# Kernel optimization log

Measured on AMD Instinct MI355X. Metric: run time of the kernel, lower is better.

The kernel has to match this reference:

```python
import jax, jax.numpy as jnp
import numpy as np

B, L, D = 2, 2048, 2048
NH, HD = 16, 128
SCALE = HD ** -0.5


def setup_inputs() -> dict:
    key = jax.random.key(0)
    ks = jax.random.split(key, 9)
    s = D ** -0.5  # roughly torch Linear init scale
    return {
        "hidden_states": jax.random.normal(ks[0], (B, L, D), dtype=jnp.float32),
        "Wq": jax.random.normal(ks[1], (NH * HD, D), dtype=jnp.float32) * s,
        "bq": jnp.zeros((NH * HD,), dtype=jnp.float32),
        "Wk": jax.random.normal(ks[2], (NH * HD, D), dtype=jnp.float32) * s,
        "bk": jnp.zeros((NH * HD,), dtype=jnp.float32),
        "Wv": jax.random.normal(ks[3], (NH * HD, D), dtype=jnp.float32) * s,
        "bv": jnp.zeros((NH * HD,), dtype=jnp.float32),
        "Wo": jax.random.normal(ks[4], (D, NH * HD), dtype=jnp.float32) * s,
        "bo": jnp.zeros((D,), dtype=jnp.float32),
    }


def reference(hidden_states, Wq, bq, Wk, bk, Wv, bv, Wo, bo):
    # projections (torch Linear: x @ W.T + b), split into heads: b s h d
    q = (hidden_states @ Wq.T + bq).reshape(B, L, NH, HD)
    k = (hidden_states @ Wk.T + bk).reshape(B, L, NH, HD)
    v = (hidden_states @ Wv.T + bv).reshape(B, L, NH, HD)
    # scores: [B, NH, L, L]
    scores = jnp.einsum("bqhd,bkhd->bhqk", q, k) * SCALE
    causal = jnp.tril(jnp.ones((L, L), dtype=bool))  # True = keep
    scores = jnp.where(causal, scores, jnp.float32(-jnp.inf))
    probs = jax.nn.softmax(scores, axis=-1)
    out = jnp.einsum("bhqk,bkhd->bqhd", probs, v).reshape(B, L, NH * HD)
    return out @ Wo.T + bo
```

## Files before the change

kernel.cpp:

```cpp
#include <hip/hip_runtime.h>

#define B_  2
#define L_  2048
#define D_  2048
#define NH_ 16
#define HD_ 128

typedef __bf16 bf16_t;
typedef __bf16 bf16x8 __attribute__((ext_vector_type(8)));
typedef __bf16 bf16x4 __attribute__((ext_vector_type(4)));
typedef float  f32x4  __attribute__((ext_vector_type(4)));

typedef const __attribute__((address_space(1))) void* gas_ptr;
typedef __attribute__((address_space(3))) void* las_ptr;

__device__ __forceinline__ void g2l16(const void* g, void* l) {
    __builtin_amdgcn_global_load_lds((gas_ptr)g, (las_ptr)l, 16, 0, 0);
}

__device__ __forceinline__ void raw_barrier() {
    asm volatile("s_barrier" ::: "memory");
}
__device__ __forceinline__ void wait_vm8() {
    asm volatile("s_waitcnt vmcnt(8)" ::: "memory");
}
__device__ __forceinline__ void wait_vm4() {
    asm volatile("s_waitcnt vmcnt(4)" ::: "memory");
}
__device__ __forceinline__ void wait_vm2() {
    asm volatile("s_waitcnt vmcnt(2)" ::: "memory");
}
__device__ __forceinline__ void wait_vm0() {
    asm volatile("s_waitcnt vmcnt(0)" ::: "memory");
}

__global__ __launch_bounds__(256) void cvt_all(const float* __restrict__ X,
                                               const float* __restrict__ Wq,
                                               const float* __restrict__ Wk,
                                               const float* __restrict__ Wv,
                                               const float* __restrict__ Wo,
                                               bf16_t* __restrict__ Xb,
                                               bf16_t* __restrict__ Wqkvb,
                                               bf16_t* __restrict__ Wob) {
    int i = blockIdx.x * 256 + threadIdx.x;
    const float* src;
    bf16_t* dst;
    int off;
    if (i < 2097152) { src = X; dst = Xb; off = i; }
    else {
        int j = i - 2097152;
        int w = j >> 20;
        off = j & 1048575;
        src = (w == 0) ? Wq : (w == 1) ? Wk : (w == 2) ? Wv : Wo;
        dst = (w == 3) ? Wob : Wqkvb + (size_t)w * 4194304;
    }
    float4 v = ((const float4*)src)[off];
    bf16x4 o;
    o[0] = (bf16_t)v.x; o[1] = (bf16_t)v.y; o[2] = (bf16_t)v.z; o[3] = (bf16_t)v.w;
    ((bf16x4*)dst)[off] = o;
}

__global__ __launch_bounds__(256) void gemm_bt(const bf16_t* __restrict__ A,
                                               const bf16_t* __restrict__ Bw,
                                               const float* __restrict__ bias,
                                               float* __restrict__ C,
                                               int M, int N, int K) {
    constexpr int BK = 32;
    __shared__ __align__(16) bf16_t smem[16384];
    const int tid  = threadIdx.x;
    const int wave = tid >> 6, lane = tid & 63;
    const int quad = lane >> 4, l16 = lane & 15;
    const int tm = blockIdx.y * 128, tn = blockIdx.x * 128;
    const int wm = (wave >> 1) * 64, wn = (wave & 1) * 64;

    const int srow = wave * 16 + (lane >> 2);
    const int scol = (lane & 3) * 8;
    const bf16_t* Ag = A  + (size_t)(tm + srow) * K + scol;
    const bf16_t* Bg = Bw + (size_t)(tn + srow) * K + scol;
    const size_t rowskip = (size_t)64 * K;

    auto stage = [&](int k0, int p) {
        bf16_t* a = smem + p * 4096 + (wave * 16) * BK;
        bf16_t* bl = smem + 8192 + p * 4096 + (wave * 16) * BK;
        g2l16(Ag + k0, a);
        g2l16(Ag + k0 + rowskip, a + 64 * BK);
        g2l16(Bg + k0, bl);
        g2l16(Bg + k0 + rowskip, bl + 64 * BK);
    };

    f32x4 acc[4][4] = {};
    const int niter = K / BK;
    stage(0, 0);

    for (int i = 0; i < niter; ++i) {
        const int p = i & 1;
        if (i + 1 < niter) { stage((i + 1) * BK, p ^ 1); wait_vm4(); }
        else wait_vm0();
        raw_barrier();

        const bf16_t* Alp = smem + p * 4096;
        const bf16_t* Blp = smem + 8192 + p * 4096;
        bf16x8 af[4], bf[4];
#pragma unroll
        for (int ii = 0; ii < 4; ++ii)
            af[ii] = *(const bf16x8*)(Alp + (wm + ii * 16 + l16) * BK + quad * 8);
#pragma unroll
        for (int j = 0; j < 4; ++j)
            bf[j] = *(const bf16x8*)(Blp + (wn + j * 16 + l16) * BK + quad * 8);
#pragma unroll
        for (int ii = 0; ii < 4; ++ii)
#pragma unroll
            for (int j = 0; j < 4; ++j)
                acc[ii][j] = __builtin_amdgcn_mfma_f32_16x16x32_bf16(af[ii], bf[j], acc[ii][j], 0, 0, 0);
        raw_barrier();
    }

#pragma unroll
    for (int j = 0; j < 4; ++j) {
        const int col = tn + wn + j * 16 + l16;
        const float bv = bias[col];
#pragma unroll
        for (int i = 0; i < 4; ++i) {
            const int row0 = tm + wm + i * 16 + quad * 4;
#pragma unroll
            for (int r = 0; r < 4; ++r)
                C[(size_t)(row0 + r) * N + col] = acc[i][j][r] + bv;
        }
    }
}

__global__ __launch_bounds__(512, 2) void gemm_qkv(const bf16_t* __restrict__ A,
                                                   const bf16_t* __restrict__ Bw,
                                                   const float* __restrict__ b0,
                                                   const float* __restrict__ b1,
                                                   const float* __restrict__ b2,
                                                   bf16_t* __restrict__ QK,
                                                   bf16_t* __restrict__ Vt) {
    constexpr int K  = D_;
    constexpr int BK = 64;
    constexpr int NT = K / BK;
    __shared__ __align__(16) bf16_t smem[65536];

    const int tid  = threadIdx.x;
    const int wave = tid >> 6, lane = tid & 63;
    const int quad = lane >> 4, l16 = lane & 15;
    const int tm = blockIdx.y * 256, tn = blockIdx.x * 256;
    const int wm = (wave >> 2) * 128;
    const int wn = (wave & 3) * 64;
    const int seg = tn >> 11;

    const int srow = tid >> 3;
    const int sg   = (tid & 7) ^ (srow & 7);
    const bf16_t* Ag = A  + (size_t)(tm + srow) * K + sg * 8;
    const bf16_t* Bg = Bw + (size_t)(tn + srow) * K + sg * 8;
    const int ldsw = wave * 512;

    auto stageA = [&](int t, int h) {
        bf16_t* l = smem + (t & 1) * 32768 + h * 8192 + ldsw;
        const bf16_t* g = Ag + (size_t)h * 128 * K + t * BK;
        g2l16(g, l);
        g2l16(g + (size_t)64 * K, l + 4096);
    };
    auto stageB = [&](int t, int h) {
        bf16_t* l = smem + (t & 1) * 32768 + 16384 + h * 8192 + ldsw;
        const bf16_t* g = Bg + (size_t)h * 128 * K + t * BK;
        g2l16(g, l);
        g2l16(g + (size_t)64 * K, l + 4096);
    };

    f32x4 acc[8][4] = {};

    stageA(0, 0); stageA(0, 1); stageB(0, 0); stageB(0, 1);

    const int abase_w = (wave >> 2) * 8192;
    const int bbase_w = 16384 + ((wave >> 1) & 1) * 8192;
    const int brow0   = (wave & 1) * 64;

    for (int t = 0; t < NT; ++t) {
        const int p = t & 1;
        const bf16_t* Ah = smem + p * 32768 + abase_w;
        const bf16_t* Bh = smem + p * 32768 + bbase_w;
        bf16x8 af[4][2], bfr[2][2], bfr2[2][2];

        raw_barrier();
        if (t + 1 < NT) { stageA(t + 1, 0); wait_vm2(); }
        else wait_vm0();
        raw_barrier();

#pragma unroll
        for (int mb = 0; mb < 4; ++mb)
#pragma unroll
            for (int ks = 0; ks < 2; ++ks) {
                const int row = mb * 16 + l16;
                af[mb][ks] = *(const bf16x8*)(Ah + row * 64 + (((ks * 4 + quad) ^ (row & 7)) << 3));
            }
#pragma unroll
        for (int nb = 0; nb < 2; ++nb)
#pragma unroll
            for (int ks = 0; ks < 2; ++ks) {
                const int row = brow0 + nb * 16 + l16;
                bfr[nb][ks] = *(const bf16x8*)(Bh + row * 64 + (((ks * 4 + quad) ^ (row & 7)) << 3));
            }
        __builtin_amdgcn_s_setprio(1);
#pragma unroll
        for (int mb = 0; mb < 4; ++mb)
#pragma unroll
            for (int nb = 0; nb < 2; ++nb)
#pragma unroll
                for (int ks = 0; ks < 2; ++ks)
                    acc[mb][nb] = __builtin_amdgcn_mfma_f32_16x16x32_bf16(af[mb][ks], bfr[nb][ks], acc[mb][nb], 0, 0, 0);
        __builtin_amdgcn_s_setprio(0);

        if (t + 1 < NT) stageA(t + 1, 1);
#pragma unroll
        for (int nb = 0; nb < 2; ++nb)
#pragma unroll
            for (int ks = 0; ks < 2; ++ks) {
                const int row = brow0 + (nb + 2) * 16 + l16;
                bfr2[nb][ks] = *(const bf16x8*)(Bh + row * 64 + (((ks * 4 + quad) ^ (row & 7)) << 3));
            }
        raw_barrier();
        __builtin_amdgcn_s_setprio(1);
#pragma unroll
        for (int mb = 0; mb < 4; ++mb)
#pragma unroll
            for (int nb = 0; nb < 2; ++nb)
#pragma unroll
                for (int ks = 0; ks < 2; ++ks)
                    acc[mb][nb + 2] = __builtin_amdgcn_mfma_f32_16x16x32_bf16(af[mb][ks], bfr2[nb][ks], acc[mb][nb + 2], 0, 0, 0);
        __builtin_amdgcn_s_setprio(0);

        if (t + 1 < NT) stageB(t + 1, 0);
#pragma unroll
        for (int mb = 0; mb < 4; ++mb)
#pragma unroll
            for (int ks = 0; ks < 2; ++ks) {
                const int row = (mb + 4) * 16 + l16;
                af[mb][ks] = *(const bf16x8*)(Ah + row * 64 + (((ks * 4 + quad) ^ (row & 7)) << 3));
            }
        raw_barrier();
        __builtin_amdgcn_s_setprio(1);
#pragma unroll
        for (int mb = 0; mb < 4; ++mb)
#pragma unroll
            for (int nb = 0; nb < 2; ++nb)
#pragma unroll
                for (int ks = 0; ks < 2; ++ks)
                    acc[mb + 4][nb + 2] = __builtin_amdgcn_mfma_f32_16x16x32_bf16(af[mb][ks], bfr2[nb][ks], acc[mb + 4][nb + 2], 0, 0, 0);
        __builtin_amdgcn_s_setprio(0);

        if (t + 1 < NT) stageB(t + 1, 1);
#pragma unroll
        for (int nb = 0; nb < 2; ++nb)
#pragma unroll
            for (int ks = 0; ks < 2; ++ks) {
                const int row = brow0 + nb * 16 + l16;
                bfr[nb][ks] = *(const bf16x8*)(Bh + row * 64 + (((ks * 4 + quad) ^ (row & 7)) << 3));
            }
        raw_barrier();
        __builtin_amdgcn_s_setprio(1);
#pragma unroll
        for (int mb = 0; mb < 4; ++mb)
#pragma unroll
            for (int nb = 0; nb < 2; ++nb)
#pragma unroll
                for (int ks = 0; ks < 2; ++ks)
                    acc[mb + 4][nb] = __builtin_amdgcn_mfma_f32_16x16x32_bf16(af[mb][ks], bfr[nb][ks], acc[mb + 4][nb], 0, 0, 0);
        __builtin_amdgcn_s_setprio(0);
    }

    if (seg < 2) {
        const float* bias = (seg == 0) ? b0 : b1;
#pragma unroll
        for (int nb = 0; nb < 4; ++nb) {
            const int col = tn + wn + nb * 16 + l16;
            const float bv = bias[col & 2047];
#pragma unroll
            for (int mb = 0; mb < 8; ++mb) {
                const int row0 = tm + wm + mb * 16 + quad * 4;
#pragma unroll
                for (int r = 0; r < 4; ++r)
                    QK[(size_t)(row0 + r) * 4096 + col] = (bf16_t)(acc[mb][nb][r] + bv);
            }
        }
    } else {
        __syncthreads();
        bf16_t* Tw = smem + wave * 8192;
        const int colbase = (tn - 4096) + wn;
#pragma unroll
        for (int nb = 0; nb < 4; ++nb) {
            const int d = nb * 16 + l16;
            const float bv = b2[colbase + d];
#pragma unroll
            for (int mb = 0; mb < 8; ++mb)
#pragma unroll
                for (int r = 0; r < 4; ++r) {
                    const int tok = mb * 16 + quad * 4 + r;
                    Tw[d * 128 + ((((tok >> 3) ^ (d & 7)) << 3) | (tok & 7))] =
                        (bf16_t)(acc[mb][nb][r] + bv);
                }
        }
        const int dl = lane;
        const int h  = (colbase + dl) >> 7;
        const int dg = (colbase + dl) & 127;
        const int b  = tm >> 11;
        const int tokbase = (tm & 2047) + wm;
        bf16_t* gp = Vt + ((size_t)(b * NH_ + h) * HD_ + dg) * L_ + tokbase;
#pragma unroll
        for (int c = 0; c < 16; ++c) {
            bf16x8 v = *(const bf16x8*)(Tw + dl * 128 + ((c ^ (dl & 7)) << 3));
            *(bf16x8*)(gp + c * 8) = v;
        }
    }
}

__global__ __launch_bounds__(256, 2) void attn_kernel(const bf16_t* __restrict__ QK,
                                                      const bf16_t* __restrict__ Vt,
                                                      bf16_t* __restrict__ Ctx) {
    constexpr float SCALE = 0.08838834764831845f;
    constexpr float MFIX  = 8.0f;
    const int bid = blockIdx.x;
    const int bh = bid & 31;
    const int qt = 15 - (bid >> 5);
    const int b = bh >> 4, h = bh & 15;
    const int tid = threadIdx.x, wave = tid >> 6, lane = tid & 63;
    const int quad = lane >> 4, l16 = lane & 15;
    const int q0 = qt * 128;

    __shared__ bf16_t Kl[2][64 * 128];
    __shared__ bf16_t Vl[2][128 * 64];
    __shared__ bf16_t Pl[4][16 * 72];

    bf16x8 qf[2][4];
#pragma unroll
    for (int s = 0; s < 2; ++s) {
        const bf16_t* qp = QK + (size_t)(b * L_ + q0 + wave * 32 + s * 16 + l16) * 4096 + h * HD_ + quad * 8;
#pragma unroll
        for (int ks = 0; ks < 4; ++ks) qf[s][ks] = *(const bf16x8*)(qp + ks * 32);
    }

    bf16x8 ones;
#pragma unroll
    for (int j = 0; j < 8; ++j) ones[j] = (bf16_t)1.0f;

    f32x4 oacc[2][8] = {};
    f32x4 lacc[2] = {};

    const bf16_t* Kg = QK + (size_t)(b * L_) * 4096 + 2048 + h * HD_;
    const bf16_t* Vg = Vt + (size_t)(bh * HD_) * L_;

    auto stage = [&](int tile, int p) {
        const bf16_t* kg = Kg + (size_t)tile * 64 * 4096;
        const bf16_t* vg = Vg + tile * 64;
#pragma unroll
        for (int c = 0; c < 4; ++c) {
            int row = c * 16 + wave * 4 + (lane >> 4);
            int gcol = ((lane & 15) ^ (row & 15)) * 8;
            g2l16(kg + (size_t)row * 4096 + gcol, &Kl[p][(c * 16 + wave * 4) * 128]);
        }
#pragma unroll
        for (int c = 0; c < 4; ++c) {
            int row = c * 32 + wave * 8 + (lane >> 3);
            int gcol = ((lane & 7) ^ (row & 7)) * 8;
            g2l16(vg + (size_t)row * L_ + gcol, &Vl[p][(c * 32 + wave * 8) * 64]);
        }
    };

    const int n = 2 * qt + 2;
    stage(0, 0);

    for (int it = 0; it < n; ++it) {
        const int p = it & 1;
        if (it + 1 < n) {
            stage(it + 1, p ^ 1);
            wait_vm8();
        } else {
            wait_vm0();
        }
        raw_barrier();

        const int kb = it * 64;
        const bool need_mask = (it >= n - 2);

        f32x4 sa[2][4] = {};
#pragma unroll
        for (int nt = 0; nt < 4; ++nt) {
            const int krow = nt * 16 + l16;
#pragma unroll
            for (int ks = 0; ks < 4; ++ks) {
                bf16x8 kf = *(const bf16x8*)(&Kl[p][krow * 128 + (((ks * 4 + quad) ^ l16) * 8)]);
                sa[0][nt] = __builtin_amdgcn_mfma_f32_16x16x32_bf16(qf[0][ks], kf, sa[0][nt], 0, 0, 0);
                sa[1][nt] = __builtin_amdgcn_mfma_f32_16x16x32_bf16(qf[1][ks], kf, sa[1][nt], 0, 0, 0);
            }
        }

        bf16x8 pf0[2], pf1[2];
#pragma unroll
        for (int nt = 0; nt < 4; ++nt)
#pragma unroll
            for (int r = 0; r < 4; ++r) {
                float sv = sa[0][nt][r] * SCALE - MFIX;
                if (need_mask) {
                    const int key = kb + nt * 16 + l16;
                    const int qq = q0 + wave * 32 + quad * 4 + r;
                    sv = (key <= qq) ? sv : -1e30f;
                }
                Pl[wave][(quad * 4 + r) * 72 + nt * 16 + l16] = (bf16_t)__expf(sv);
            }
        pf0[0] = *(const bf16x8*)(&Pl[wave][l16 * 72 + quad * 8]);
        pf0[1] = *(const bf16x8*)(&Pl[wave][l16 * 72 + 32 + quad * 8]);

#pragma unroll
        for (int nt = 0; nt < 4; ++nt)
#pragma unroll
            for (int r = 0; r < 4; ++r) {
                float sv = sa[1][nt][r] * SCALE - MFIX;
                if (need_mask) {
                    const int key = kb + nt * 16 + l16;
                    const int qq = q0 + wave * 32 + 16 + quad * 4 + r;
                    sv = (key <= qq) ? sv : -1e30f;
                }
                Pl[wave][(quad * 4 + r) * 72 + nt * 16 + l16] = (bf16_t)__expf(sv);
            }
        pf1[0] = *(const bf16x8*)(&Pl[wave][l16 * 72 + quad * 8]);
        pf1[1] = *(const bf16x8*)(&Pl[wave][l16 * 72 + 32 + quad * 8]);

        lacc[0] = __builtin_amdgcn_mfma_f32_16x16x32_bf16(pf0[0], ones, lacc[0], 0, 0, 0);
        lacc[0] = __builtin_amdgcn_mfma_f32_16x16x32_bf16(pf0[1], ones, lacc[0], 0, 0, 0);
        lacc[1] = __builtin_amdgcn_mfma_f32_16x16x32_bf16(pf1[0], ones, lacc[1], 0, 0, 0);
        lacc[1] = __builtin_amdgcn_mfma_f32_16x16x32_bf16(pf1[1], ones, lacc[1], 0, 0, 0);

#pragma unroll
        for (int dt = 0; dt < 8; ++dt) {
            const int drow = dt * 16 + l16;
#pragma unroll
            for (int ks = 0; ks < 2; ++ks) {
                bf16x8 vf = *(const bf16x8*)(&Vl[p][drow * 64 + (((ks * 4 + quad) ^ (drow & 7)) * 8)]);
                oacc[0][dt] = __builtin_amdgcn_mfma_f32_16x16x32_bf16(pf0[ks], vf, oacc[0][dt], 0, 0, 0);
                oacc[1][dt] = __builtin_amdgcn_mfma_f32_16x16x32_bf16(pf1[ks], vf, oacc[1][dt], 0, 0, 0);
            }
        }
        raw_barrier();
    }

#pragma unroll
    for (int s = 0; s < 2; ++s)
#pragma unroll
        for (int r = 0; r < 4; ++r) {
            const float inv = 1.0f / lacc[s][r];
            const int q = q0 + wave * 32 + s * 16 + quad * 4 + r;
            bf16_t* cp = Ctx + (size_t)(b * L_ + q) * 2048 + h * HD_;
#pragma unroll
            for (int dt = 0; dt < 8; ++dt)
                cp[dt * 16 + l16] = (bf16_t)(oacc[s][dt][r] * inv);
        }
}

extern "C" void kernel_launch(void* const* d_in, const int* in_sizes, int n_in,
                              void* d_out, int out_size, void* d_ws, size_t ws_size,
                              hipStream_t stream) {
    const float* X  = (const float*)d_in[0];
    const float* Wq = (const float*)d_in[1];
    const float* bq = (const float*)d_in[2];
    const float* Wk = (const float*)d_in[3];
    const float* bk = (const float*)d_in[4];
    const float* Wv = (const float*)d_in[5];
    const float* bv = (const float*)d_in[6];
    const float* Wo = (const float*)d_in[7];
    const float* bo = (const float*)d_in[8];
    float* out = (float*)d_out;

    char* ws = (char*)d_ws;
    bf16_t* Xb   = (bf16_t*)(ws);
    bf16_t* Ctx  = (bf16_t*)(ws);
    bf16_t* Wqkv = (bf16_t*)(ws + 16777216);
    bf16_t* Wob  = (bf16_t*)(ws + 41943040);
    bf16_t* QKb  = (bf16_t*)(ws + 50331648);
    bf16_t* Vtb  = (bf16_t*)(ws + 83886080);

    cvt_all<<<24576, 256, 0, stream>>>(X, Wq, Wk, Wv, Wo, Xb, Wqkv, Wob);

    gemm_qkv<<<dim3(24, 16), 512, 0, stream>>>(Xb, Wqkv, bq, bk, bv, QKb, Vtb);

    attn_kernel<<<dim3(512), 256, 0, stream>>>(QKb, Vtb, Ctx);

    gemm_bt<<<dim3(16, 32), 256, 0, stream>>>(Ctx, Wob, bo, out,
                                              B_ * L_, D_, D_);
}
```

Measured before the change: 371.1 us.

## Split fused QKV GEMM into separate QK and V GEMM kernels

The single 24x16-block QKV projection GEMM is split into a Q/K GEMM using 256x256 tiles (256 blocks) and a new V GEMM using 256x128 tiles (256 blocks) with its own transposed-output epilogue. The goal is to fix wave quantization: 384 large blocks on 256 CUs leave a partial second wave, while two 256-block launches fill the device more evenly. The cost is an extra kernel launch, smaller tiles with less reuse in the V GEMM, and A being re-read by both kernels.

```diff
diff --git a/kernel.cpp b/kernel.cpp
--- a/kernel.cpp
+++ b/kernel.cpp
@@ -129,13 +129,11 @@
     }
 }
 
-__global__ __launch_bounds__(512, 2) void gemm_qkv(const bf16_t* __restrict__ A,
-                                                   const bf16_t* __restrict__ Bw,
-                                                   const float* __restrict__ b0,
-                                                   const float* __restrict__ b1,
-                                                   const float* __restrict__ b2,
-                                                   bf16_t* __restrict__ QK,
-                                                   bf16_t* __restrict__ Vt) {
+__global__ __launch_bounds__(512, 2) void gemm_qk(const bf16_t* __restrict__ A,
+                                                  const bf16_t* __restrict__ Bw,
+                                                  const float* __restrict__ b0,
+                                                  const float* __restrict__ b1,
+                                                  bf16_t* __restrict__ QK) {
     constexpr int K  = D_;
     constexpr int BK = 64;
     constexpr int NT = K / BK;
@@ -269,48 +267,160 @@
         __builtin_amdgcn_s_setprio(0);
     }
 
-    if (seg < 2) {
-        const float* bias = (seg == 0) ? b0 : b1;
-#pragma unroll
-        for (int nb = 0; nb < 4; ++nb) {
-            const int col = tn + wn + nb * 16 + l16;
-            const float bv = bias[col & 2047];
-#pragma unroll
-            for (int mb = 0; mb < 8; ++mb) {
-                const int row0 = tm + wm + mb * 16 + quad * 4;
-#pragma unroll
-                for (int r = 0; r < 4; ++r)
-                    QK[(size_t)(row0 + r) * 4096 + col] = (bf16_t)(acc[mb][nb][r] + bv);
-            }
-        }
-    } else {
-        __syncthreads();
-        bf16_t* Tw = smem + wave * 8192;
-        const int colbase = (tn - 4096) + wn;
-#pragma unroll
-        for (int nb = 0; nb < 4; ++nb) {
-            const int d = nb * 16 + l16;
-            const float bv = b2[colbase + d];
-#pragma unroll
-            for (int mb = 0; mb < 8; ++mb)
-#pragma unroll
-                for (int r = 0; r < 4; ++r) {
-                    const int tok = mb * 16 + quad * 4 + r;
-                    Tw[d * 128 + ((((tok >> 3) ^ (d & 7)) << 3) | (tok & 7))] =
-                        (bf16_t)(acc[mb][nb][r] + bv);
-                }
-        }
-        const int dl = lane;
-        const int h  = (colbase + dl) >> 7;
-        const int dg = (colbase + dl) & 127;
-        const int b  = tm >> 11;
-        const int tokbase = (tm & 2047) + wm;
-        bf16_t* gp = Vt + ((size_t)(b * NH_ + h) * HD_ + dg) * L_ + tokbase;
-#pragma unroll
-        for (int c = 0; c < 16; ++c) {
-            bf16x8 v = *(const bf16x8*)(Tw + dl * 128 + ((c ^ (dl & 7)) << 3));
-            *(bf16x8*)(gp + c * 8) = v;
-        }
+    const float* bias = (seg == 0) ? b0 : b1;
+#pragma unroll
+    for (int nb = 0; nb < 4; ++nb) {
+        const int col = tn + wn + nb * 16 + l16;
+        const float bv = bias[col & 2047];
+#pragma unroll
+        for (int mb = 0; mb < 8; ++mb) {
+            const int row0 = tm + wm + mb * 16 + quad * 4;
+#pragma unroll
+            for (int r = 0; r < 4; ++r)
+                QK[(size_t)(row0 + r) * 4096 + col] = (bf16_t)(acc[mb][nb][r] + bv);
+        }
+    }
+}
+
+__global__ __launch_bounds__(512, 2) void gemm_v(const bf16_t* __restrict__ A,
+                                                 const bf16_t* __restrict__ Bv,
+                                                 const float* __restrict__ b2,
+                                                 bf16_t* __restrict__ Vt) {
+    constexpr int K  = D_;
+    constexpr int BK = 64;
+    constexpr int NT = K / BK;
+    __shared__ __align__(16) bf16_t smem[49152];
+
+    const int tid  = threadIdx.x;
+    const int wave = tid >> 6, lane = tid & 63;
+    const int quad = lane >> 4, l16 = lane & 15;
+    const int hx = blockIdx.x;
+    const int tm = blockIdx.y * 256;
+    const int wm = (wave >> 1) * 64;
+    const int wn = (wave & 1) * 64;
+
+    const int srow = tid >> 3;
+    const int sg   = (tid & 7) ^ (srow & 7);
+    const bf16_t* Ag = A  + (size_t)(tm + srow) * K + sg * 8;
+    const bf16_t* Bg = Bv + (size_t)(hx * 128 + srow) * K + sg * 8;
+    const int ldsw = wave * 512;
+
+    auto stageVA = [&](int t, int q) {
+        bf16_t* l = smem + (t & 1) * 24576 + q * 4096 + ldsw;
+        g2l16(Ag + (size_t)q * 64 * K + t * BK, l);
+    };
+    auto stageVB = [&](int t, int q) {
+        bf16_t* l = smem + (t & 1) * 24576 + 16384 + q * 4096 + ldsw;
+        g2l16(Bg + (size_t)q * 64 * K + t * BK, l);
+    };
+
+    f32x4 acc[4][4] = {};
+
+    stageVA(0, 0); stageVA(0, 1); stageVA(0, 2); stageVA(0, 3);
+    stageVB(0, 0); stageVB(0, 1);
+
+    for (int t = 0; t < NT; ++t) {
+        const int p = t & 1;
+        const bf16_t* Ah = smem + p * 24576;
+        const bf16_t* Bl = smem + p * 24576 + 16384;
+        bf16x8 af0[4], af1[4], bf0[2], bf1[2], bf2[2], bf3[2];
+
+        raw_barrier();
+        if (t + 1 < NT) { stageVA(t + 1, 0); stageVA(t + 1, 1); wait_vm2(); }
+        else wait_vm0();
+        raw_barrier();
+
+#pragma unroll
+        for (int mb = 0; mb < 4; ++mb) {
+            const int row = wm + mb * 16 + l16;
+            af0[mb] = *(const bf16x8*)(Ah + row * 64 + ((quad ^ (row & 7)) << 3));
+        }
+#pragma unroll
+        for (int nb = 0; nb < 2; ++nb) {
+            const int row = wn + nb * 16 + l16;
+            bf0[nb] = *(const bf16x8*)(Bl + row * 64 + ((quad ^ (row & 7)) << 3));
+        }
+        __builtin_amdgcn_s_setprio(1);
+#pragma unroll
+        for (int mb = 0; mb < 4; ++mb)
+#pragma unroll
+            for (int nb = 0; nb < 2; ++nb)
+                acc[mb][nb] = __builtin_amdgcn_mfma_f32_16x16x32_bf16(af0[mb], bf0[nb], acc[mb][nb], 0, 0, 0);
+        __builtin_amdgcn_s_setprio(0);
+
+        if (t + 1 < NT) { stageVA(t + 1, 2); stageVB(t + 1, 0); }
+#pragma unroll
+        for (int nb = 0; nb < 2; ++nb) {
+            const int row = wn + (nb + 2) * 16 + l16;
+            bf1[nb] = *(const bf16x8*)(Bl + row * 64 + ((quad ^ (row & 7)) << 3));
+        }
+        raw_barrier();
+        __builtin_amdgcn_s_setprio(1);
+#pragma unroll
+        for (int mb = 0; mb < 4; ++mb)
+#pragma unroll
+            for (int nb = 0; nb < 2; ++nb)
+                acc[mb][nb + 2] = __builtin_amdgcn_mfma_f32_16x16x32_bf16(af0[mb], bf1[nb], acc[mb][nb + 2], 0, 0, 0);
+        __builtin_amdgcn_s_setprio(0);
+
+        if (t + 1 < NT) { stageVA(t + 1, 3); stageVB(t + 1, 1); }
+#pragma unroll
+        for (int mb = 0; mb < 4; ++mb) {
+            const int row = wm + mb * 16 + l16;
+            af1[mb] = *(const bf16x8*)(Ah + row * 64 + (((4 + quad) ^ (row & 7)) << 3));
+        }
+#pragma unroll
+        for (int nb = 0; nb < 2; ++nb) {
+            const int row = wn + (nb + 2) * 16 + l16;
+            bf2[nb] = *(const bf16x8*)(Bl + row * 64 + (((4 + quad) ^ (row & 7)) << 3));
+        }
+        raw_barrier();
+        __builtin_amdgcn_s_setprio(1);
+#pragma unroll
+        for (int mb = 0; mb < 4; ++mb)
+#pragma unroll
+            for (int nb = 0; nb < 2; ++nb)
+                acc[mb][nb + 2] = __builtin_amdgcn_mfma_f32_16x16x32_bf16(af1[mb], bf2[nb], acc[mb][nb + 2], 0, 0, 0);
+        __builtin_amdgcn_s_setprio(0);
+
+#pragma unroll
+        for (int nb = 0; nb < 2; ++nb) {
+            const int row = wn + nb * 16 + l16;
+            bf3[nb] = *(const bf16x8*)(Bl + row * 64 + (((4 + quad) ^ (row & 7)) << 3));
+        }
+        raw_barrier();
+        __builtin_amdgcn_s_setprio(1);
+#pragma unroll
+        for (int mb = 0; mb < 4; ++mb)
+#pragma unroll
+            for (int nb = 0; nb < 2; ++nb)
+                acc[mb][nb] = __builtin_amdgcn_mfma_f32_16x16x32_bf16(af1[mb], bf3[nb], acc[mb][nb], 0, 0, 0);
+        __builtin_amdgcn_s_setprio(0);
+    }
+
+    __syncthreads();
+    bf16_t* Tw = smem + wave * 4096;
+    const int b = tm >> 11;
+    const int tokbase = tm & 2047;
+#pragma unroll
+    for (int nb = 0; nb < 4; ++nb) {
+        const int dloc = nb * 16 + l16;
+        const float bv = b2[hx * 128 + wn + dloc];
+#pragma unroll
+        for (int mb = 0; mb < 4; ++mb)
+#pragma unroll
+            for (int r = 0; r < 4; ++r) {
+                const int tokl = mb * 16 + quad * 4 + r;
+                Tw[dloc * 64 + ((((tokl >> 3) ^ (dloc & 7)) << 3) | (tokl & 7))] =
+                    (bf16_t)(acc[mb][nb][r] + bv);
+            }
+    }
+    const int dl = lane;
+    bf16_t* gp = Vt + ((size_t)(b * NH_ + hx) * HD_ + wn + dl) * L_ + tokbase + wm;
+#pragma unroll
+    for (int c = 0; c < 8; ++c) {
+        bf16x8 v = *(const bf16x8*)(Tw + dl * 64 + ((c ^ (dl & 7)) << 3));
+        *(bf16x8*)(gp + c * 8) = v;
     }
 }
 
@@ -480,7 +590,9 @@
 
     cvt_all<<<24576, 256, 0, stream>>>(X, Wq, Wk, Wv, Wo, Xb, Wqkv, Wob);
 
-    gemm_qkv<<<dim3(24, 16), 512, 0, stream>>>(Xb, Wqkv, bq, bk, bv, QKb, Vtb);
+    gemm_qk<<<dim3(16, 16), 512, 0, stream>>>(Xb, Wqkv, bq, bk, QKb);
+
+    gemm_v<<<dim3(16, 16), 512, 0, stream>>>(Xb, Wqkv + 8388608, bv, Vtb);
 
     attn_kernel<<<dim3(512), 256, 0, stream>>>(QKb, Vtb, Ctx);
 
```

Measured after the change: 359.8 us. 1.03x faster.
